# Kernel optimization log

Measured on AMD Instinct MI355X. Metric: run time of the kernel, lower is better.

## Reference

```python
import jax, jax.numpy as jnp
import numpy as np

D_MODEL = 2048
N_HEADS = 16
HEAD_DIM = D_MODEL // N_HEADS


def _rotate_half(x):
    # matches torch: x1 = x[..., ::2], x2 = x[..., 1::2]; cat(-x2, x1)
    x1 = x[..., ::2]
    x2 = x[..., 1::2]
    return jnp.concatenate((-x2, x1), axis=-1)


def _rope_sin_cos(seq_len, dtype):
    # NOTE: module builds RoPE tables over the FULL d_model, then truncates to head_dim.
    inv_freq = 1.0 / (10000.0 ** (np.arange(0, D_MODEL, 2, dtype=np.float32) / D_MODEL))
    pos = np.arange(seq_len, dtype=np.float32)
    freqs = pos[:, None] * inv_freq[None, :]          # [S, d_model/2]
    sin = jnp.asarray(np.sin(freqs)[:, :HEAD_DIM], dtype=dtype)  # [S, head_dim]
    cos = jnp.asarray(np.cos(freqs)[:, :HEAD_DIM], dtype=dtype)
    return sin[None, None], cos[None, None]           # [1,1,S,head_dim]


def setup_inputs() -> dict:
    key = jax.random.key(0)
    ks = jax.random.split(key, 11)
    B, S = 2, 2048
    sc = 1.0 / np.sqrt(D_MODEL)
    inp = {
        "query": jax.random.normal(ks[0], (B, S, D_MODEL), jnp.float32),
        "key": jax.random.normal(ks[1], (B, S, D_MODEL), jnp.float32),
        "value": jax.random.normal(ks[2], (B, S, D_MODEL), jnp.float32),
        "Wq": jax.random.normal(ks[3], (D_MODEL, D_MODEL), jnp.float32) * sc,
        "bq": jnp.zeros((D_MODEL,), jnp.float32),
        "Wk": jax.random.normal(ks[4], (D_MODEL, D_MODEL), jnp.float32) * sc,
        "bk": jnp.zeros((D_MODEL,), jnp.float32),
        "Wv": jax.random.normal(ks[5], (D_MODEL, D_MODEL), jnp.float32) * sc,
        "bv": jnp.zeros((D_MODEL,), jnp.float32),
        "Wo": jax.random.normal(ks[6], (D_MODEL, D_MODEL), jnp.float32) * sc,
        "bo": jnp.zeros((D_MODEL,), jnp.float32),
    }
    return inp


def reference(query, key, value, Wq, bq, Wk, bk, Wv, bv, Wo, bo):
    B, S, _ = query.shape

    def split_heads(x):
        return x.reshape(B, S, N_HEADS, HEAD_DIM).transpose(0, 2, 1, 3)  # [B,H,S,d_k]

    Q = split_heads(query @ Wq.T + bq)
    K = split_heads(key @ Wk.T + bk)
    V = split_heads(value @ Wv.T + bv)

    sin, cos = _rope_sin_cos(S, Q.dtype)
    Q = Q * cos + _rotate_half(Q) * sin
    K = K * cos + _rotate_half(K) * sin

    scores = jnp.einsum("bhqd,bhkd->bhqk", Q, K) / np.sqrt(HEAD_DIM)
    probs = jax.nn.softmax(scores, axis=-1)  # dropout is identity at eval
    context = jnp.einsum("bhqk,bhkd->bhqd", probs, V)
    out = context.transpose(0, 2, 1, 3).reshape(B, S, D_MODEL)
    return out @ Wo.T + bo
```

## Files before the change

kernel.cpp:

```cpp
#include <hip/hip_runtime.h>
#include <hip/hip_bf16.h>

#define D_MODEL 2048
#define SEQ     2048
#define BATCH   2
#define NH      16
#define HD      128
#define MROWS   (BATCH*SEQ)

typedef __attribute__((ext_vector_type(8)))  short bf16x8;
typedef __attribute__((ext_vector_type(4)))  float f32x4;
typedef __attribute__((ext_vector_type(16))) float f32x16;
typedef __attribute__((ext_vector_type(4)))  unsigned int u32x4;

static __device__ __forceinline__ void lds16(const void* g, void* l) {
    __builtin_amdgcn_global_load_lds(
        (const __attribute__((address_space(1))) void*)g,
        (__attribute__((address_space(3))) void*)l,
        16, 0, 0);
}

static __device__ __forceinline__ unsigned int pk2(float a, float b) {
    const unsigned int lo = __bfloat16_as_ushort(__float2bfloat16(a));
    const unsigned int hh = __bfloat16_as_ushort(__float2bfloat16(b));
    return lo | (hh << 16);
}
static __device__ __forceinline__ unsigned short bfu(float a) {
    return __bfloat16_as_ushort(__float2bfloat16(a));
}

__global__ __launch_bounds__(256) void cvt_all(
    const float* __restrict__ q,  const float* __restrict__ k,  const float* __restrict__ v,
    const float* __restrict__ wq, const float* __restrict__ wk, const float* __restrict__ wv,
    const float* __restrict__ wo,
    unsigned short* __restrict__ qb, unsigned short* __restrict__ kb, unsigned short* __restrict__ vb,
    unsigned short* __restrict__ wqb, unsigned short* __restrict__ wkb,
    unsigned short* __restrict__ wvb, unsigned short* __restrict__ wob)
{
    const int b = blockIdx.x;
    const float* src; unsigned short* dst; int idx;
    if (b < 24576) {
        const int s = b >> 13;
        idx = (b & 8191)*256 + threadIdx.x;
        src = (s==0) ? q : (s==1) ? k : v;
        dst = (s==0) ? qb : (s==1) ? kb : vb;
    } else {
        const int bb = b - 24576;
        const int s = bb >> 12;
        idx = (bb & 4095)*256 + threadIdx.x;
        src = (s==0) ? wq : (s==1) ? wk : (s==2) ? wv : wo;
        dst = (s==0) ? wqb : (s==1) ? wkb : (s==2) ? wvb : wob;
    }
    const float4 a = ((const float4*)src)[idx];
    ushort4 o;
    o.x = bfu(a.x); o.y = bfu(a.y); o.z = bfu(a.z); o.w = bfu(a.w);
    ((ushort4*)dst)[idx] = o;
}

__global__ __launch_bounds__(256) void rope_table(float* __restrict__ tab)
{
    const int i = blockIdx.x*256 + threadIdx.x;
    const int s = i >> 7, d = i & 127;
    const float invf = expf(-(float)d * (9.210340371976184f / 1024.0f));
    const float f = (float)s * invf;
    tab[(size_t)s*256 + d]       = cosf(f);
    tab[(size_t)s*256 + 128 + d] = sinf(f);
}

__global__ __launch_bounds__(256, 2) void gemm_qkv_fused(
    const __hip_bfloat16* __restrict__ Aq,
    const __hip_bfloat16* __restrict__ Ak,
    const __hip_bfloat16* __restrict__ Av,
    const __hip_bfloat16* __restrict__ Wq, const __hip_bfloat16* __restrict__ Wk,
    const __hip_bfloat16* __restrict__ Wv,
    const float* __restrict__ bq, const float* __restrict__ bk, const float* __restrict__ bv,
    const float* __restrict__ tab,
    __hip_bfloat16* __restrict__ Qp, __hip_bfloat16* __restrict__ Kp,
    __hip_bfloat16* __restrict__ Vt)
{
    __shared__ char smem[65536];
    __hip_bfloat16* As = (__hip_bfloat16*)smem;
    __hip_bfloat16* Bs = (__hip_bfloat16*)(smem + 32768);

    const int K    = D_MODEL;
    const int x    = blockIdx.x & 7;
    const int r    = blockIdx.x >> 3;
    const int bn   = r >> 2;
    const int bm   = x*4 + (r & 3);
    const int mat  = bn >> 4;
    const int hd   = bn & 15;
    const __hip_bfloat16* A  = (mat==0) ? Aq : (mat==1) ? Ak : Av;
    const __hip_bfloat16* W  = (mat==0) ? Wq : (mat==1) ? Wk : Wv;
    const float*          bi = (mat==0) ? bq : (mat==1) ? bk : bv;

    const int tid  = threadIdx.x;
    const int lane = tid & 63;
    const int w    = tid >> 6;
    const int wr   = (w >> 1) * 64;
    const int wc   = (w & 1) * 64;
    const int l15  = lane & 15, l4 = lane >> 4;

    const int srow = w*32 + (lane>>2);
    const __hip_bfloat16* ga = A + (size_t)(bm*128 + srow)*K + (lane&3)*8;
    const __hip_bfloat16* gb = W + (size_t)(hd*128 + srow)*K + (lane&3)*8;

#define GSTAGE(Q_, KT_) do {                                               \
        lds16(ga + (KT_),                &As[(Q_)*4096 + (w*32)*32]);      \
        lds16(ga + (KT_) + (size_t)16*K, &As[(Q_)*4096 + (w*32+16)*32]);   \
        lds16(gb + (KT_),                &Bs[(Q_)*4096 + (w*32)*32]);      \
        lds16(gb + (KT_) + (size_t)16*K, &Bs[(Q_)*4096 + (w*32+16)*32]);   \
    } while (0)

    f32x4 acc[4][4] = {};
    const int NT = K >> 5;

    GSTAGE(0, 0);
    GSTAGE(1, 32);
    asm volatile("s_waitcnt vmcnt(4)" ::: "memory");
    __builtin_amdgcn_s_barrier();

    for (int t = 0; t < NT; ++t) {
        const int q = t & 3;
        if (t + 2 < NT) GSTAGE((t+2)&3, (t+2)*32);
        bf16x8 af[4], bfr[4];
        #pragma unroll
        for (int i = 0; i < 4; i++) {
            af[i]  = *(const bf16x8*)&As[q*4096 + (wr + i*16 + l15)*32 + l4*8];
            bfr[i] = *(const bf16x8*)&Bs[q*4096 + (wc + i*16 + l15)*32 + l4*8];
        }
        __builtin_amdgcn_s_setprio(1);
        #pragma unroll
        for (int i = 0; i < 4; i++)
            #pragma unroll
            for (int j = 0; j < 4; j++)
                acc[i][j] = __builtin_amdgcn_mfma_f32_16x16x32_bf16(af[i], bfr[j], acc[i][j], 0, 0, 0);
        __builtin_amdgcn_s_setprio(0);
        if (t + 2 < NT) {
            asm volatile("s_waitcnt vmcnt(4)" ::: "memory");
            __builtin_amdgcn_s_barrier();
        } else if (t + 1 < NT) {
            asm volatile("s_waitcnt vmcnt(0)" ::: "memory");
            __builtin_amdgcn_s_barrier();
        }
    }
#undef GSTAGE

    __syncthreads();
    float* Ct = (float*)smem;

    #pragma unroll
    for (int i = 0; i < 4; i++) {
        #pragma unroll
        for (int j = 0; j < 4; j++) {
            const int col = wc + j*16 + l15;
            const float bvv = bi[hd*128 + col];
            #pragma unroll
            for (int rr = 0; rr < 4; rr++) {
                const int row = wr + i*16 + l4*4 + rr;
                Ct[row*128 + (col ^ (row & 31))] = acc[i][j][rr] + bvv;
            }
        }
    }
    __syncthreads();

    const int grow0 = bm*128;
    const int bb    = grow0 >> 11;
    const int s0    = grow0 & (SEQ-1);

    if (mat < 2) {
        __hip_bfloat16* Out = (mat==0) ? Qp : Kp;
        #pragma unroll
        for (int p = 0; p < 16; p++) {
            const int rl = p*8 + (tid>>5);
            const int c4 = (tid&31)*4;
            const int kx = rl & 31;
            const float* tc = tab + (size_t)(s0 + rl)*256;
            float o[4];
            #pragma unroll
            for (int i2 = 0; i2 < 4; i2++) {
                const int d  = c4 + i2;
                const float xx = Ct[rl*128 + (d ^ kx)];
                const int   pd = (d < 64) ? (2*d + 1) : (2*d - 128);
                const float xp = Ct[rl*128 + (pd ^ kx)];
                const float cs = tc[d], sn = tc[128 + d];
                o[i2] = (d < 64) ? (xx*cs - xp*sn) : (xx*cs + xp*sn);
            }
            ushort4 pkd;
            pkd.x = bfu(o[0]); pkd.y = bfu(o[1]); pkd.z = bfu(o[2]); pkd.w = bfu(o[3]);
            *(ushort4*)(Out + (size_t)(grow0 + rl)*D_MODEL + hd*HD + c4) = pkd;
        }
    } else {
        unsigned short* vt = (unsigned short*)Vt;
        #pragma unroll
        for (int p = 0; p < 16; p++) {
            const int d  = p*8 + (tid>>5);
            const int s4 = (tid&31)*4;
            float o[4];
            #pragma unroll
            for (int i2 = 0; i2 < 4; i2++) {
                const int sr = s4 + i2;
                o[i2] = Ct[sr*128 + (d ^ (sr & 31))];
            }
            ushort4 pkd;
            pkd.x = bfu(o[0]); pkd.y = bfu(o[1]); pkd.z = bfu(o[2]); pkd.w = bfu(o[3]);
            *(ushort4*)(vt + ((size_t)(bb*16 + hd)*HD + d)*SEQ + s0 + s4) = pkd;
        }
    }
}

__global__ __launch_bounds__(256, 2) void gemm_bt_bias_f32(
    const __hip_bfloat16* __restrict__ A,
    const __hip_bfloat16* __restrict__ W,
    const float* __restrict__ bias,
    float* __restrict__ C,
    const int M, const int N, const int K)
{
    __shared__ __hip_bfloat16 As[4][128*32];
    __shared__ __hip_bfloat16 Bs[4][128*32];
    const int x    = blockIdx.x & 7;
    const int r    = blockIdx.x >> 3;
    const int bn   = r >> 2;
    const int bm   = x*4 + (r & 3);
    const int tid  = threadIdx.x;
    const int lane = tid & 63;
    const int w    = tid >> 6;
    const int wr   = (w >> 1) * 64;
    const int wc   = (w & 1) * 64;
    const int l15  = lane & 15, l4 = lane >> 4;

    const int srow = w*32 + (lane>>2);
    const __hip_bfloat16* ga = A + (size_t)(bm*128 + srow)*K + (lane&3)*8;
    const __hip_bfloat16* gb = W + (size_t)(bn*128 + srow)*K + (lane&3)*8;

#define GSTAGE(Q_, KT_) do {                                          \
        lds16(ga + (KT_),                &As[Q_][(w*32)*32]);         \
        lds16(ga + (KT_) + (size_t)16*K, &As[Q_][(w*32+16)*32]);      \
        lds16(gb + (KT_),                &Bs[Q_][(w*32)*32]);         \
        lds16(gb + (KT_) + (size_t)16*K, &Bs[Q_][(w*32+16)*32]);      \
    } while (0)

    f32x4 acc[4][4] = {};
    const int NT = K >> 5;

    GSTAGE(0, 0);
    GSTAGE(1, 32);
    asm volatile("s_waitcnt vmcnt(4)" ::: "memory");
    __builtin_amdgcn_s_barrier();

    for (int t = 0; t < NT; ++t) {
        const int q = t & 3;
        if (t + 2 < NT) GSTAGE((t+2)&3, (t+2)*32);
        bf16x8 af[4], bfr[4];
        #pragma unroll
        for (int i = 0; i < 4; i++) {
            af[i]  = *(const bf16x8*)&As[q][(wr + i*16 + l15)*32 + l4*8];
            bfr[i] = *(const bf16x8*)&Bs[q][(wc + i*16 + l15)*32 + l4*8];
        }
        __builtin_amdgcn_s_setprio(1);
        #pragma unroll
        for (int i = 0; i < 4; i++)
            #pragma unroll
            for (int j = 0; j < 4; j++)
                acc[i][j] = __builtin_amdgcn_mfma_f32_16x16x32_bf16(af[i], bfr[j], acc[i][j], 0, 0, 0);
        __builtin_amdgcn_s_setprio(0);
        if (t + 2 < NT) {
            asm volatile("s_waitcnt vmcnt(4)" ::: "memory");
            __builtin_amdgcn_s_barrier();
        } else if (t + 1 < NT) {
            asm volatile("s_waitcnt vmcnt(0)" ::: "memory");
            __builtin_amdgcn_s_barrier();
        }
    }
#undef GSTAGE

    float bv[4];
    #pragma unroll
    for (int j = 0; j < 4; j++)
        bv[j] = bias[bn*128 + wc + j*16 + l15];
    #pragma unroll
    for (int i = 0; i < 4; i++) {
        #pragma unroll
        for (int j = 0; j < 4; j++) {
            const int col = bn*128 + wc + j*16 + l15;
            #pragma unroll
            for (int rr = 0; rr < 4; rr++) {
                const int row = bm*128 + wr + i*16 + l4*4 + rr;
                C[(size_t)row*N + col] = acc[i][j][rr] + bv[j];
            }
        }
    }
}

__global__ __launch_bounds__(256, 2) void flash_attn(
    const __hip_bfloat16* __restrict__ Qg,
    const __hip_bfloat16* __restrict__ Kg,
    const __hip_bfloat16* __restrict__ Vtg,
    __hip_bfloat16* __restrict__ ctx)
{
    __shared__ __hip_bfloat16 Ks[2][64*128];
    __shared__ __hip_bfloat16 Vs[2][128*64];

    const int tid  = threadIdx.x;
    const int w    = tid >> 6;
    const int lane = tid & 63;
    const int l31  = lane & 31;
    const int hi   = lane >> 5;
    const bool hib = (hi != 0);

    const int bid0 = blockIdx.x;
    const int bid  = (bid0 & 7)*64 + (bid0 >> 3);
    const int bh   = bid >> 4;
    const int qt   = bid & 15;
    const int bi   = bh >> 4, h = bh & 15;
    const int q0   = qt * 128;

    const float SC = 0.08838834764831845f;

    bf16x8 aq[8];
    {
        const __hip_bfloat16* qp =
            Qg + (size_t)(bi*SEQ + q0 + w*32 + l31)*D_MODEL + h*HD + hi*8;
        #pragma unroll
        for (int ds = 0; ds < 8; ds++) aq[ds] = *(const bf16x8*)(qp + ds*16);
    }

#define STAGE(NB, KV) do {                                                              \
        _Pragma("unroll")                                                               \
        for (int i_ = 0; i_ < 4; i_++) {                                                \
            const int kr_ = w*16 + i_*4 + (lane>>4);                                    \
            lds16(Kg + (size_t)(bi*SEQ + (KV) + kr_)*D_MODEL + h*HD                     \
                      + (((lane&15) ^ (kr_&15))*8),                                     \
                  &Ks[NB][(w*16 + i_*4)*128]);                                          \
        }                                                                               \
        _Pragma("unroll")                                                               \
        for (int i_ = 0; i_ < 4; i_++) {                                                \
            const int vr_ = w*32 + i_*8 + (lane>>3);                                    \
            lds16(Vtg + ((size_t)bh*HD + vr_)*SEQ + (KV)                                \
                      + (((lane&7) ^ (lane>>3))*8),                                     \
                  &Vs[NB][(w*32 + i_*8)*64]);                                           \
        }                                                                               \
    } while (0)

    f32x16 o0 = {}, o1 = {}, o2 = {}, o3 = {};
    float m_run = -1e30f, l_run = 0.0f;

    STAGE(0, 0);

    for (int t = 0; t < SEQ/64; t++) {
        const int cb = t & 1;
        __syncthreads();
        if (t < SEQ/64 - 1) STAGE(cb^1, (t+1)*64);

        f32x16 p0 = {}, p1 = {};
        #pragma unroll
        for (int ds = 0; ds < 8; ds++) {
            const int sl = ((ds*2 + hi) ^ (lane&15)) * 8;
            const bf16x8 k0 = *(const bf16x8*)&Ks[cb][l31*128 + sl];
            const bf16x8 k1 = *(const bf16x8*)&Ks[cb][(32 + l31)*128 + sl];
            p0 = __builtin_amdgcn_mfma_f32_32x32x16_bf16(k0, aq[ds], p0, 0, 0, 0);
            p1 = __builtin_amdgcn_mfma_f32_32x32x16_bf16(k1, aq[ds], p1, 0, 0, 0);
        }

        float pm = fmaxf(p0[0], p1[0]);
        #pragma unroll
        for (int r = 1; r < 16; r++) pm = fmaxf(pm, fmaxf(p0[r], p1[r]));
        pm = fmaxf(pm, __shfl_xor(pm, 32));

        if (!__all(pm <= m_run + 90.509667f)) {
            const float mnew = fmaxf(m_run, pm);
            const float al = __expf((m_run - mnew) * SC);
            l_run *= al;
            m_run = mnew;
            float alr[16];
            #pragma unroll
            for (int r = 0; r < 16; r++)
                alr[r] = __shfl(al, (r&3) + 8*(r>>2) + (hib ? 4 : 0));
            #pragma unroll
            for (int r = 0; r < 16; r++) {
                o0[r] *= alr[r]; o1[r] *= alr[r]; o2[r] *= alr[r]; o3[r] *= alr[r];
            }
        }

        #pragma unroll
        for (int r = 0; r < 16; r++) {
            p0[r] = __expf((p0[r] - m_run) * SC);
            p1[r] = __expf((p1[r] - m_run) * SC);
        }
        float rs = 0.0f;
        #pragma unroll
        for (int r = 0; r < 16; r++) rs += p0[r] + p1[r];
        rs += __shfl_xor(rs, 32);
        l_run += rs;

#define PV_STEP(PF, KS) do {                                                            \
            const unsigned int A0_ = pk2(PF[8*((KS)&1)+0], PF[8*((KS)&1)+1]);           \
            const unsigned int A1_ = pk2(PF[8*((KS)&1)+2], PF[8*((KS)&1)+3]);           \
            const unsigned int B0_ = pk2(PF[8*((KS)&1)+4], PF[8*((KS)&1)+5]);           \
            const unsigned int B1_ = pk2(PF[8*((KS)&1)+6], PF[8*((KS)&1)+7]);           \
            const unsigned int s0_ = hib ? A0_ : B0_;                                   \
            const unsigned int s1_ = hib ? A1_ : B1_;                                   \
            const unsigned int r0_ = (unsigned int)__shfl_xor((int)s0_, 32);            \
            const unsigned int r1_ = (unsigned int)__shfl_xor((int)s1_, 32);            \
            u32x4 au_;                                                                  \
            au_.x = hib ? r0_ : A0_;  au_.y = hib ? r1_ : A1_;                          \
            au_.z = hib ? B0_ : r0_;  au_.w = hib ? B1_ : r1_;                          \
            const bf16x8 pa_ = *(const bf16x8*)&au_;                                    \
            const int ko_ = (((KS)*2 + hi) ^ (lane&7)) * 8;                             \
            o0 = __builtin_amdgcn_mfma_f32_32x32x16_bf16(pa_,                           \
                     *(const bf16x8*)&Vs[cb][(  0 + l31)*64 + ko_], o0, 0, 0, 0);       \
            o1 = __builtin_amdgcn_mfma_f32_32x32x16_bf16(pa_,                           \
                     *(const bf16x8*)&Vs[cb][( 32 + l31)*64 + ko_], o1, 0, 0, 0);       \
            o2 = __builtin_amdgcn_mfma_f32_32x32x16_bf16(pa_,                           \
                     *(const bf16x8*)&Vs[cb][( 64 + l31)*64 + ko_], o2, 0, 0, 0);       \
            o3 = __builtin_amdgcn_mfma_f32_32x32x16_bf16(pa_,                           \
                     *(const bf16x8*)&Vs[cb][( 96 + l31)*64 + ko_], o3, 0, 0, 0);       \
        } while (0)

        PV_STEP(p0, 0); PV_STEP(p0, 1); PV_STEP(p1, 2); PV_STEP(p1, 3);
#undef PV_STEP
    }

    const float inv = 1.0f / l_run;
    float invr[16];
    #pragma unroll
    for (int r = 0; r < 16; r++)
        invr[r] = __shfl(inv, (r&3) + 8*(r>>2) + (hib ? 4 : 0));

    #pragma unroll
    for (int r = 0; r < 16; r++) {
        const int qr = q0 + w*32 + (r&3) + 8*(r>>2) + (hib ? 4 : 0);
        __hip_bfloat16* cp = ctx + (size_t)(bi*SEQ + qr)*D_MODEL + h*HD + l31;
        cp[0]  = __float2bfloat16(o0[r] * invr[r]);
        cp[32] = __float2bfloat16(o1[r] * invr[r]);
        cp[64] = __float2bfloat16(o2[r] * invr[r]);
        cp[96] = __float2bfloat16(o3[r] * invr[r]);
    }
#undef STAGE
}

extern "C" void kernel_launch(void* const* d_in, const int* in_sizes, int n_in,
                              void* d_out, int out_size, void* d_ws, size_t ws_size,
                              hipStream_t stream)
{
    const float* query = (const float*)d_in[0];
    const float* key   = (const float*)d_in[1];
    const float* value = (const float*)d_in[2];
    const float* Wq    = (const float*)d_in[3];
    const float* bq    = (const float*)d_in[4];
    const float* Wk    = (const float*)d_in[5];
    const float* bk    = (const float*)d_in[6];
    const float* Wv    = (const float*)d_in[7];
    const float* bv    = (const float*)d_in[8];
    const float* Wo    = (const float*)d_in[9];
    const float* bo    = (const float*)d_in[10];
    float* out = (float*)d_out;

    char* ws = (char*)d_ws;
    const size_t MB = 1024*1024;
    __hip_bfloat16* qb  = (__hip_bfloat16*)(ws);
    __hip_bfloat16* kbuf= (__hip_bfloat16*)(ws + 16*MB);
    __hip_bfloat16* vbuf= (__hip_bfloat16*)(ws + 32*MB);
    __hip_bfloat16* Qp  = (__hip_bfloat16*)(ws + 48*MB);
    __hip_bfloat16* Kp  = (__hip_bfloat16*)(ws + 64*MB);
    __hip_bfloat16* Vt  = (__hip_bfloat16*)(ws + 80*MB);
    __hip_bfloat16* ctx = (__hip_bfloat16*)(ws + 96*MB);
    __hip_bfloat16* Wqb = (__hip_bfloat16*)(ws + 112*MB);
    __hip_bfloat16* Wkb = (__hip_bfloat16*)(ws + 120*MB);
    __hip_bfloat16* Wvb = (__hip_bfloat16*)(ws + 128*MB);
    __hip_bfloat16* Wob = (__hip_bfloat16*)(ws + 136*MB);
    float*          tab = (float*)         (ws + 144*MB);

    cvt_all<<<40960, 256, 0, stream>>>(query, key, value, Wq, Wk, Wv, Wo,
        (unsigned short*)qb, (unsigned short*)kbuf, (unsigned short*)vbuf,
        (unsigned short*)Wqb, (unsigned short*)Wkb, (unsigned short*)Wvb,
        (unsigned short*)Wob);

    rope_table<<<SEQ*HD/256, 256, 0, stream>>>(tab);

    gemm_qkv_fused<<<(MROWS/128)*48, 256, 0, stream>>>(
        qb, kbuf, vbuf, Wqb, Wkb, Wvb, bq, bk, bv, tab, Qp, Kp, Vt);

    flash_attn<<<BATCH*NH*(SEQ/128), 256, 0, stream>>>(Qp, Kp, Vt, ctx);

    gemm_bt_bias_f32<<<(MROWS/128)*(D_MODEL/128), 256, 0, stream>>>(
        ctx, Wob, bo, out, MROWS, D_MODEL, D_MODEL);
}
```

Before: 312.4 us.

## Rewrite QKV and output GEMMs with 128x256 tiles, 8 waves, triple-buffered LDS

Both projection GEMMs move to a shared mainloop with 512 threads (2x4 waves), 128x256 output tiles, K-step 64 and a 3-stage LDS ring of 48KB per stage with XOR-swizzled slots. The loop splits each K-step into four MFMA phases and interleaves the next stage's global-to-LDS loads between them, with barriers and setprio around each phase. The aim is more operand reuse per byte loaded, fewer LDS bank conflicts, and better overlap of loads with MFMA. In exchange it uses 144KB of LDS per block, so only one block fits per CU, and the extra barriers add synchronisation cost. The QKV epilogue is adapted so each block covers two heads.

```diff
diff --git a/kernel.cpp b/kernel.cpp
--- a/kernel.cpp
+++ b/kernel.cpp
@@ -67,7 +67,99 @@
     tab[(size_t)s*256 + 128 + d] = sinf(f);
 }
 
-__global__ __launch_bounds__(256, 2) void gemm_qkv_fused(
+#define GV2_DECLS                                                             \
+    const int tid  = threadIdx.x;                                             \
+    const int lane = tid & 63;                                                \
+    const int w    = tid >> 6;                                      \
+    const int wm   = w >> 2;                                        \
+    const int wn   = w & 3;                                         \
+    const int l15  = lane & 15;                                               \
+    const int l4   = lane >> 4;                                     \
+    const int lrow = lane >> 3;                                     \
+    const int lslot= (lane & 7) ^ lrow;         \
+    const int sl0  = ((l4)     ^ (l15 & 7)) << 4;   \
+    const int sl1  = ((4 + l4) ^ (l15 & 7)) << 4;                   \
+    const int rA0m = (wm*64 +  0 + l15)*128, rA1m = (wm*64 + 16 + l15)*128,   \
+              rA2m = (wm*64 + 32 + l15)*128, rA3m = (wm*64 + 48 + l15)*128;   \
+    const int rB0m = 16384 + (wn*64 +  0 + l15)*128,                          \
+              rB1m = 16384 + (wn*64 + 16 + l15)*128,                          \
+              rB2m = 16384 + (wn*64 + 32 + l15)*128,                          \
+              rB3m = 16384 + (wn*64 + 48 + l15)*128;
+
+#define SA(Q_, KT_, I_) lds16(Ag + (size_t)(arow0 + (I_)*64 + w*8 + lrow)*2048 \
+                                  + (KT_)*64 + lslot*8,                        \
+                              smem + (Q_)*49152 + ((I_)*64 + w*8)*128)
+#define SB(Q_, KT_, J_) lds16(Wg + (size_t)(wrow0 + (J_)*64 + w*8 + lrow)*2048 \
+                                  + (KT_)*64 + lslot*8,                        \
+                              smem + (Q_)*49152 + 16384 + ((J_)*64 + w*8)*128)
+
+#define MF(AF, BF, I_, J_) acc[I_][J_] = \
+    __builtin_amdgcn_mfma_f32_16x16x32_bf16(AF, BF, acc[I_][J_], 0, 0, 0)
+
+#define GV2_KLOOP                                                              \
+    f32x4 acc[4][4] = {};                                                      \
+    { SA(0,0,0); SA(0,0,1); SB(0,0,0); SB(0,0,1); SB(0,0,2); SB(0,0,3);        \
+      SA(1,1,0); SA(1,1,1); SB(1,1,0); SB(1,1,1); SB(1,1,2); SB(1,1,3); }      \
+    asm volatile("s_waitcnt vmcnt(6)" ::: "memory");                           \
+    __builtin_amdgcn_s_barrier();                                              \
+    int bi3 = 0, q2 = 2;                                                       \
+    for (int t = 0; t < 32; ++t) {                                             \
+        const char* cb = smem + bi3*49152;                                     \
+        const bool st = (t + 2 < 32);                                          \
+                                                                       \
+        bf16x8 a0 = *(const bf16x8*)(cb + rA0m + sl0);                         \
+        bf16x8 a1 = *(const bf16x8*)(cb + rA1m + sl0);                         \
+        bf16x8 a2 = *(const bf16x8*)(cb + rA2m + sl0);                         \
+        bf16x8 a3 = *(const bf16x8*)(cb + rA3m + sl0);                         \
+        bf16x8 b0 = *(const bf16x8*)(cb + rB0m + sl0);                         \
+        bf16x8 b1 = *(const bf16x8*)(cb + rB1m + sl0);                         \
+        if (st) { SA(q2, t+2, 0); SA(q2, t+2, 1); }                            \
+        __builtin_amdgcn_s_barrier();                                          \
+        __builtin_amdgcn_s_setprio(1);                                         \
+        MF(a0,b0,0,0); MF(a1,b0,1,0); MF(a2,b0,2,0); MF(a3,b0,3,0);            \
+        MF(a0,b1,0,1); MF(a1,b1,1,1); MF(a2,b1,2,1); MF(a3,b1,3,1);            \
+        __builtin_amdgcn_s_setprio(0);                                         \
+        __builtin_amdgcn_s_barrier();                                          \
+                                                                       \
+        bf16x8 b2 = *(const bf16x8*)(cb + rB2m + sl0);                         \
+        bf16x8 b3 = *(const bf16x8*)(cb + rB3m + sl0);                         \
+        if (st) { SB(q2, t+2, 0); SB(q2, t+2, 1); }                            \
+        __builtin_amdgcn_s_barrier();                                          \
+        __builtin_amdgcn_s_setprio(1);                                         \
+        MF(a0,b2,0,2); MF(a1,b2,1,2); MF(a2,b2,2,2); MF(a3,b2,3,2);            \
+        MF(a0,b3,0,3); MF(a1,b3,1,3); MF(a2,b3,2,3); MF(a3,b3,3,3);            \
+        __builtin_amdgcn_s_setprio(0);                                         \
+        __builtin_amdgcn_s_barrier();                                          \
+                                                                       \
+        a0 = *(const bf16x8*)(cb + rA0m + sl1);                                \
+        a1 = *(const bf16x8*)(cb + rA1m + sl1);                                \
+        a2 = *(const bf16x8*)(cb + rA2m + sl1);                                \
+        a3 = *(const bf16x8*)(cb + rA3m + sl1);                                \
+        b0 = *(const bf16x8*)(cb + rB0m + sl1);                                \
+        b1 = *(const bf16x8*)(cb + rB1m + sl1);                                \
+        if (st) { SB(q2, t+2, 2); SB(q2, t+2, 3); }                            \
+        __builtin_amdgcn_s_barrier();                                          \
+        __builtin_amdgcn_s_setprio(1);                                         \
+        MF(a0,b0,0,0); MF(a1,b0,1,0); MF(a2,b0,2,0); MF(a3,b0,3,0);            \
+        MF(a0,b1,0,1); MF(a1,b1,1,1); MF(a2,b1,2,1); MF(a3,b1,3,1);            \
+        __builtin_amdgcn_s_setprio(0);                                         \
+        __builtin_amdgcn_s_barrier();                                          \
+                                                                       \
+        b2 = *(const bf16x8*)(cb + rB2m + sl1);                                \
+        b3 = *(const bf16x8*)(cb + rB3m + sl1);                                \
+        if (st)            { asm volatile("s_waitcnt vmcnt(6)" ::: "memory"); }\
+        else if (t+1 < 32) { asm volatile("s_waitcnt vmcnt(0)" ::: "memory"); }\
+        __builtin_amdgcn_s_barrier();                                          \
+        __builtin_amdgcn_s_setprio(1);                                         \
+        MF(a0,b2,0,2); MF(a1,b2,1,2); MF(a2,b2,2,2); MF(a3,b2,3,2);            \
+        MF(a0,b3,0,3); MF(a1,b3,1,3); MF(a2,b3,2,3); MF(a3,b3,3,3);            \
+        __builtin_amdgcn_s_setprio(0);                                         \
+        __builtin_amdgcn_s_barrier();                                          \
+        bi3 = (bi3 == 2) ? 0 : bi3 + 1;                                        \
+        q2  = (q2  == 2) ? 0 : q2  + 1;                                        \
+    }
+
+__global__ __launch_bounds__(512) void gemm_qkv_v2(
     const __hip_bfloat16* __restrict__ Aq,
     const __hip_bfloat16* __restrict__ Ak,
     const __hip_bfloat16* __restrict__ Av,
@@ -78,72 +170,22 @@
     __hip_bfloat16* __restrict__ Qp, __hip_bfloat16* __restrict__ Kp,
     __hip_bfloat16* __restrict__ Vt)
 {
-    __shared__ char smem[65536];
-    __hip_bfloat16* As = (__hip_bfloat16*)smem;
-    __hip_bfloat16* Bs = (__hip_bfloat16*)(smem + 32768);
-
-    const int K    = D_MODEL;
-    const int x    = blockIdx.x & 7;
-    const int r    = blockIdx.x >> 3;
-    const int bn   = r >> 2;
-    const int bm   = x*4 + (r & 3);
-    const int mat  = bn >> 4;
-    const int hd   = bn & 15;
-    const __hip_bfloat16* A  = (mat==0) ? Aq : (mat==1) ? Ak : Av;
-    const __hip_bfloat16* W  = (mat==0) ? Wq : (mat==1) ? Wk : Wv;
+    __shared__ char smem[147456];
+
+    const int xcd = blockIdx.x & 7;
+    const int rr2 = blockIdx.x >> 3;
+    const int bm  = xcd*4 + (rr2 & 3);
+    const int bn  = rr2 >> 2;
+    const int mat = bn >> 3;
+    const int hd2 = bn & 7;
+    const __hip_bfloat16* Ag = (mat==0) ? Aq : (mat==1) ? Ak : Av;
+    const __hip_bfloat16* Wg = (mat==0) ? Wq : (mat==1) ? Wk : Wv;
     const float*          bi = (mat==0) ? bq : (mat==1) ? bk : bv;
-
-    const int tid  = threadIdx.x;
-    const int lane = tid & 63;
-    const int w    = tid >> 6;
-    const int wr   = (w >> 1) * 64;
-    const int wc   = (w & 1) * 64;
-    const int l15  = lane & 15, l4 = lane >> 4;
-
-    const int srow = w*32 + (lane>>2);
-    const __hip_bfloat16* ga = A + (size_t)(bm*128 + srow)*K + (lane&3)*8;
-    const __hip_bfloat16* gb = W + (size_t)(hd*128 + srow)*K + (lane&3)*8;
-
-#define GSTAGE(Q_, KT_) do {                                               \
-        lds16(ga + (KT_),                &As[(Q_)*4096 + (w*32)*32]);      \
-        lds16(ga + (KT_) + (size_t)16*K, &As[(Q_)*4096 + (w*32+16)*32]);   \
-        lds16(gb + (KT_),                &Bs[(Q_)*4096 + (w*32)*32]);      \
-        lds16(gb + (KT_) + (size_t)16*K, &Bs[(Q_)*4096 + (w*32+16)*32]);   \
-    } while (0)
-
-    f32x4 acc[4][4] = {};
-    const int NT = K >> 5;
-
-    GSTAGE(0, 0);
-    GSTAGE(1, 32);
-    asm volatile("s_waitcnt vmcnt(4)" ::: "memory");
-    __builtin_amdgcn_s_barrier();
-
-    for (int t = 0; t < NT; ++t) {
-        const int q = t & 3;
-        if (t + 2 < NT) GSTAGE((t+2)&3, (t+2)*32);
-        bf16x8 af[4], bfr[4];
-        #pragma unroll
-        for (int i = 0; i < 4; i++) {
-            af[i]  = *(const bf16x8*)&As[q*4096 + (wr + i*16 + l15)*32 + l4*8];
-            bfr[i] = *(const bf16x8*)&Bs[q*4096 + (wc + i*16 + l15)*32 + l4*8];
-        }
-        __builtin_amdgcn_s_setprio(1);
-        #pragma unroll
-        for (int i = 0; i < 4; i++)
-            #pragma unroll
-            for (int j = 0; j < 4; j++)
-                acc[i][j] = __builtin_amdgcn_mfma_f32_16x16x32_bf16(af[i], bfr[j], acc[i][j], 0, 0, 0);
-        __builtin_amdgcn_s_setprio(0);
-        if (t + 2 < NT) {
-            asm volatile("s_waitcnt vmcnt(4)" ::: "memory");
-            __builtin_amdgcn_s_barrier();
-        } else if (t + 1 < NT) {
-            asm volatile("s_waitcnt vmcnt(0)" ::: "memory");
-            __builtin_amdgcn_s_barrier();
-        }
-    }
-#undef GSTAGE
+    const int arow0 = bm*128;
+    const int wrow0 = hd2*256;
+
+    GV2_DECLS
+    GV2_KLOOP
 
     __syncthreads();
     float* Ct = (float*)smem;
@@ -152,12 +194,12 @@
     for (int i = 0; i < 4; i++) {
         #pragma unroll
         for (int j = 0; j < 4; j++) {
-            const int col = wc + j*16 + l15;
-            const float bvv = bi[hd*128 + col];
+            const int col = wn*64 + j*16 + l15;
+            const float bvv = bi[hd2*256 + col];
             #pragma unroll
             for (int rr = 0; rr < 4; rr++) {
-                const int row = wr + i*16 + l4*4 + rr;
-                Ct[row*128 + (col ^ (row & 31))] = acc[i][j][rr] + bvv;
+                const int row = wm*64 + i*16 + l4*4 + rr;
+                Ct[row*256 + (col ^ (row & 31))] = acc[i][j][rr] + bvv;
             }
         }
     }
@@ -171,121 +213,78 @@
         __hip_bfloat16* Out = (mat==0) ? Qp : Kp;
         #pragma unroll
         for (int p = 0; p < 16; p++) {
-            const int rl = p*8 + (tid>>5);
-            const int c4 = (tid&31)*4;
+            const int rl = p*8 + (tid>>6);
             const int kx = rl & 31;
+            const int c0 = (tid & 63)*4;
             const float* tc = tab + (size_t)(s0 + rl)*256;
             float o[4];
             #pragma unroll
             for (int i2 = 0; i2 < 4; i2++) {
-                const int d  = c4 + i2;
-                const float xx = Ct[rl*128 + (d ^ kx)];
+                const int c  = c0 + i2;
+                const int h2 = c >> 7;
+                const int d  = c & 127;
+                const float xx = Ct[rl*256 + (c ^ kx)];
                 const int   pd = (d < 64) ? (2*d + 1) : (2*d - 128);
-                const float xp = Ct[rl*128 + (pd ^ kx)];
+                const float xp = Ct[rl*256 + ((h2*128 + pd) ^ kx)];
                 const float cs = tc[d], sn = tc[128 + d];
                 o[i2] = (d < 64) ? (xx*cs - xp*sn) : (xx*cs + xp*sn);
             }
             ushort4 pkd;
             pkd.x = bfu(o[0]); pkd.y = bfu(o[1]); pkd.z = bfu(o[2]); pkd.w = bfu(o[3]);
-            *(ushort4*)(Out + (size_t)(grow0 + rl)*D_MODEL + hd*HD + c4) = pkd;
+            *(ushort4*)(Out + (size_t)(grow0 + rl)*D_MODEL + hd2*256 + c0) = pkd;
         }
     } else {
         unsigned short* vt = (unsigned short*)Vt;
         #pragma unroll
         for (int p = 0; p < 16; p++) {
-            const int d  = p*8 + (tid>>5);
-            const int s4 = (tid&31)*4;
+            const int c  = p*16 + (tid>>5);
+            const int h2 = c >> 7;
+            const int d  = c & 127;
+            const int sb = (tid & 31)*4;
             float o[4];
             #pragma unroll
             for (int i2 = 0; i2 < 4; i2++) {
-                const int sr = s4 + i2;
-                o[i2] = Ct[sr*128 + (d ^ (sr & 31))];
+                const int sr = sb + i2;
+                o[i2] = Ct[sr*256 + (c ^ (sr & 31))];
             }
             ushort4 pkd;
             pkd.x = bfu(o[0]); pkd.y = bfu(o[1]); pkd.z = bfu(o[2]); pkd.w = bfu(o[3]);
-            *(ushort4*)(vt + ((size_t)(bb*16 + hd)*HD + d)*SEQ + s0 + s4) = pkd;
-        }
-    }
-}
-
-__global__ __launch_bounds__(256, 2) void gemm_bt_bias_f32(
-    const __hip_bfloat16* __restrict__ A,
-    const __hip_bfloat16* __restrict__ W,
+            *(ushort4*)(vt + ((size_t)(bb*16 + hd2*2 + h2)*HD + d)*SEQ + s0 + sb) = pkd;
+        }
+    }
+}
+
+__global__ __launch_bounds__(512) void gemm_out_v2(
+    const __hip_bfloat16* __restrict__ Ag,
+    const __hip_bfloat16* __restrict__ Wg,
     const float* __restrict__ bias,
-    float* __restrict__ C,
-    const int M, const int N, const int K)
-{
-    __shared__ __hip_bfloat16 As[4][128*32];
-    __shared__ __hip_bfloat16 Bs[4][128*32];
-    const int x    = blockIdx.x & 7;
-    const int r    = blockIdx.x >> 3;
-    const int bn   = r >> 2;
-    const int bm   = x*4 + (r & 3);
-    const int tid  = threadIdx.x;
-    const int lane = tid & 63;
-    const int w    = tid >> 6;
-    const int wr   = (w >> 1) * 64;
-    const int wc   = (w & 1) * 64;
-    const int l15  = lane & 15, l4 = lane >> 4;
-
-    const int srow = w*32 + (lane>>2);
-    const __hip_bfloat16* ga = A + (size_t)(bm*128 + srow)*K + (lane&3)*8;
-    const __hip_bfloat16* gb = W + (size_t)(bn*128 + srow)*K + (lane&3)*8;
-
-#define GSTAGE(Q_, KT_) do {                                          \
-        lds16(ga + (KT_),                &As[Q_][(w*32)*32]);         \
-        lds16(ga + (KT_) + (size_t)16*K, &As[Q_][(w*32+16)*32]);      \
-        lds16(gb + (KT_),                &Bs[Q_][(w*32)*32]);         \
-        lds16(gb + (KT_) + (size_t)16*K, &Bs[Q_][(w*32+16)*32]);      \
-    } while (0)
-
-    f32x4 acc[4][4] = {};
-    const int NT = K >> 5;
-
-    GSTAGE(0, 0);
-    GSTAGE(1, 32);
-    asm volatile("s_waitcnt vmcnt(4)" ::: "memory");
-    __builtin_amdgcn_s_barrier();
-
-    for (int t = 0; t < NT; ++t) {
-        const int q = t & 3;
-        if (t + 2 < NT) GSTAGE((t+2)&3, (t+2)*32);
-        bf16x8 af[4], bfr[4];
-        #pragma unroll
-        for (int i = 0; i < 4; i++) {
-            af[i]  = *(const bf16x8*)&As[q][(wr + i*16 + l15)*32 + l4*8];
-            bfr[i] = *(const bf16x8*)&Bs[q][(wc + i*16 + l15)*32 + l4*8];
-        }
-        __builtin_amdgcn_s_setprio(1);
-        #pragma unroll
-        for (int i = 0; i < 4; i++)
-            #pragma unroll
-            for (int j = 0; j < 4; j++)
-                acc[i][j] = __builtin_amdgcn_mfma_f32_16x16x32_bf16(af[i], bfr[j], acc[i][j], 0, 0, 0);
-        __builtin_amdgcn_s_setprio(0);
-        if (t + 2 < NT) {
-            asm volatile("s_waitcnt vmcnt(4)" ::: "memory");
-            __builtin_amdgcn_s_barrier();
-        } else if (t + 1 < NT) {
-            asm volatile("s_waitcnt vmcnt(0)" ::: "memory");
-            __builtin_amdgcn_s_barrier();
-        }
-    }
-#undef GSTAGE
-
-    float bv[4];
+    float* __restrict__ C)
+{
+    __shared__ char smem[147456];
+
+    const int xcd = blockIdx.x & 7;
+    const int r2  = blockIdx.x >> 3;
+    const int bm  = xcd*4 + (r2 & 3);
+    const int bn  = r2 >> 2;
+    const int arow0 = bm*128;
+    const int wrow0 = bn*256;
+
+    GV2_DECLS
+    GV2_KLOOP
+
+    float bvv[4];
     #pragma unroll
     for (int j = 0; j < 4; j++)
-        bv[j] = bias[bn*128 + wc + j*16 + l15];
+        bvv[j] = bias[bn*256 + wn*64 + j*16 + l15];
     #pragma unroll
     for (int i = 0; i < 4; i++) {
         #pragma unroll
         for (int j = 0; j < 4; j++) {
-            const int col = bn*128 + wc + j*16 + l15;
+            const int col = bn*256 + wn*64 + j*16 + l15;
             #pragma unroll
             for (int rr = 0; rr < 4; rr++) {
-                const int row = bm*128 + wr + i*16 + l4*4 + rr;
-                C[(size_t)row*N + col] = acc[i][j][rr] + bv[j];
+                const int row = bm*128 + wm*64 + i*16 + l4*4 + rr;
+                C[(size_t)row*D_MODEL + col] = acc[i][j][rr] + bvv[j];
             }
         }
     }
@@ -477,11 +476,10 @@
 
     rope_table<<<SEQ*HD/256, 256, 0, stream>>>(tab);
 
-    gemm_qkv_fused<<<(MROWS/128)*48, 256, 0, stream>>>(
+    gemm_qkv_v2<<<768, 512, 0, stream>>>(
         qb, kbuf, vbuf, Wqb, Wkb, Wvb, bq, bk, bv, tab, Qp, Kp, Vt);
 
     flash_attn<<<BATCH*NH*(SEQ/128), 256, 0, stream>>>(Qp, Kp, Vt, ctx);
 
-    gemm_bt_bias_f32<<<(MROWS/128)*(D_MODEL/128), 256, 0, stream>>>(
-        ctx, Wob, bo, out, MROWS, D_MODEL, D_MODEL);
-}
+    gemm_out_v2<<<256, 512, 0, stream>>>(ctx, Wob, bo, out);
+}
```

Measured after the change: 310.0 us. Within noise of the previous version (-0.8%).
